# Kernel tuning notes

Measured on AMD Instinct MI355X. Metric: run time of the kernel, lower is better.

## Reference

```python
import jax, jax.numpy as jnp
import numpy as np

EPS = 1e-7  # tf.keras.backend.epsilon()
DEGREE = 5
SCALE_BASE = 1.0
SCALE_LEGENDRE = 1.0


def legendre_basis(x, degree):
    # min/max normalization over the feature axis -> x_norm in [-1, 1]
    x_min = jnp.min(x, axis=-1, keepdims=True)
    x_max = jnp.max(x, axis=-1, keepdims=True)
    x_norm = 2.0 * (x - x_min) / (x_max - x_min + EPS) - 1.0
    polys = [jnp.ones_like(x_norm), x_norm]
    for n in range(2, degree + 1):
        p_n = ((2 * n - 1) * x_norm * polys[-1] - (n - 1) * polys[-2]) / n
        polys.append(p_n)
    return jnp.stack(polys, axis=-1)  # [b, i, degree+1]


def setup_inputs() -> dict:
    key = jax.random.key(0)
    k1, k2, k3 = jax.random.split(key, 3)
    b, i, o, d = 4096, 1024, 1024, DEGREE + 1
    x = jax.random.normal(k1, (b, i), dtype=jnp.float32)
    # HeUniform: limit = sqrt(6 / fan_in)
    lim_b = np.sqrt(6.0 / i)
    base_weight = jax.random.uniform(k2, (i, o), dtype=jnp.float32, minval=-lim_b, maxval=lim_b)
    legendre_weight = jax.random.uniform(k3, (i, o, d), dtype=jnp.float32, minval=-lim_b, maxval=lim_b)
    return {"x": x, "base_weight": base_weight, "legendre_weight": legendre_weight}


def reference(x, base_weight, legendre_weight):
    base_output = jax.nn.silu(x @ base_weight)  # [b, o]
    basis = legendre_basis(x, DEGREE)  # [b, i, d]
    # 'bi,iod,bid->bo' == fold x into the basis then contract (i, d)
    xb = x[..., None] * basis  # [b, i, d]
    legendre_output = jnp.einsum('bid,iod->bo', xb, legendre_weight)
    return SCALE_BASE * base_output + SCALE_LEGENDRE * legendre_output
```

## Files before the change

kernel.cpp:

```cpp
#include <hip/hip_runtime.h>
#include <stdint.h>

typedef unsigned short u16;
typedef unsigned int   u32;
typedef __attribute__((ext_vector_type(8)))  short bhalf8;
typedef __attribute__((ext_vector_type(16))) float f32x16;

#define B_ROWS 4096
#define I_DIM  1024
#define O_DIM  1024
#define N_D    6
#define K_LEG  (I_DIM * N_D)

#define BM 256
#define BN 256
#define BK 32
#define NU 56
#define SLOT_BYTES 32768
#define LDS_BYTES  131072

__device__ __forceinline__ u16 f2b(float f) {
  u32 u = __float_as_uint(f);
  return (u16)((u + 0x7fffu + ((u >> 16) & 1u)) >> 16);
}

__device__ __forceinline__ void gld_lds16(const void* g, void* l) {
  __builtin_amdgcn_global_load_lds(
      (const __attribute__((address_space(1))) u32*)(uintptr_t)g,
      (__attribute__((address_space(3))) u32*)(u32)(uintptr_t)l, 16, 0, 0);
}

#define RS 201
__global__ void k_prep_w(const float* __restrict__ bw, const float* __restrict__ lw,
                         u16* __restrict__ Bb, u16* __restrict__ Bl) {
  __shared__ float t[32 * RS];
  if (blockIdx.x < 1024) {
    const int bx = blockIdx.x & 31, by = blockIdx.x >> 5;
    const int i0 = by * 32, o0 = bx * 32;
    const int c = threadIdx.x & 31, r0 = threadIdx.x >> 5;
    #pragma unroll
    for (int k = 0; k < 4; ++k) {
      int r = r0 + k * 8;
      t[r * 33 + c] = bw[(size_t)(i0 + r) * O_DIM + o0 + c];
    }
    __syncthreads();
    #pragma unroll
    for (int k = 0; k < 4; ++k) {
      int r = r0 + k * 8;
      Bb[(size_t)(o0 + r) * I_DIM + i0 + c] = f2b(t[c * 33 + r]);
    }
  } else {
    const int blk = blockIdx.x - 1024;
    const int bx = blk & 31, by = blk >> 5;
    const int i0 = by * 32, o0 = bx * 32;
    for (int q = threadIdx.x; q < 32 * 48; q += 256) {
      int ri = q / 48, s4 = q % 48;
      float4 v = *(const float4*)(lw + (size_t)(i0 + ri) * (O_DIM * N_D) + o0 * N_D + s4 * 4);
      float* p = t + ri * RS + s4 * 4;
      p[0] = v.x; p[1] = v.y; p[2] = v.z; p[3] = v.w;
    }
    __syncthreads();
    for (int q = threadIdx.x; q < 32 * 96; q += 256) {
      int ro = q / 96, k = q % 96;
      int e0 = 2 * k, e1 = 2 * k + 1;
      float v0 = t[(e0 / 6) * RS + ro * 6 + (e0 % 6)];
      float v1 = t[(e1 / 6) * RS + ro * 6 + (e1 % 6)];
      u32* dst = (u32*)(Bl + (size_t)(o0 + ro) * K_LEG + i0 * N_D);
      dst[k] = (u32)f2b(v0) | ((u32)f2b(v1) << 16);
    }
  }
}

__global__ void k_prep_basis(const float* __restrict__ x,
                             u16* __restrict__ Ab, u16* __restrict__ Al) {
  int b = blockIdx.x;
  int t = threadIdx.x;
  float4 v = ((const float4*)(x + (size_t)b * I_DIM))[t];
  float mn = fminf(fminf(v.x, v.y), fminf(v.z, v.w));
  float mx = fmaxf(fmaxf(v.x, v.y), fmaxf(v.z, v.w));
  #pragma unroll
  for (int off = 32; off > 0; off >>= 1) {
    mn = fminf(mn, __shfl_xor(mn, off, 64));
    mx = fmaxf(mx, __shfl_xor(mx, off, 64));
  }
  __shared__ float smn[4], smx[4];
  if ((t & 63) == 0) { smn[t >> 6] = mn; smx[t >> 6] = mx; }
  __syncthreads();
  mn = fminf(fminf(smn[0], smn[1]), fminf(smn[2], smn[3]));
  mx = fmaxf(fmaxf(smx[0], smx[1]), fmaxf(smx[2], smx[3]));
  float sc = 2.0f / (mx - mn + 1e-7f);

  float xs[4] = {v.x, v.y, v.z, v.w};
  u32 lb[12];
  #pragma unroll
  for (int e = 0; e < 4; ++e) {
    float xv = xs[e];
    float xn = (xv - mn) * sc - 1.0f;
    float p0 = 1.0f, p1 = xn;
    float p2 = (3.0f * xn * p1 - 1.0f * p0) * (1.0f / 2.0f);
    float p3 = (5.0f * xn * p2 - 2.0f * p1) * (1.0f / 3.0f);
    float p4 = (7.0f * xn * p3 - 3.0f * p2) * (1.0f / 4.0f);
    float p5 = (9.0f * xn * p4 - 4.0f * p3) * (1.0f / 5.0f);
    lb[e * 3 + 0] = (u32)f2b(xv * p0) | ((u32)f2b(xv * p1) << 16);
    lb[e * 3 + 1] = (u32)f2b(xv * p2) | ((u32)f2b(xv * p3) << 16);
    lb[e * 3 + 2] = (u32)f2b(xv * p4) | ((u32)f2b(xv * p5) << 16);
  }
  u32 a0 = (u32)f2b(xs[0]) | ((u32)f2b(xs[1]) << 16);
  u32 a1 = (u32)f2b(xs[2]) | ((u32)f2b(xs[3]) << 16);
  *(uint2*)(Ab + (size_t)b * I_DIM + t * 4) = make_uint2(a0, a1);
  uint4* dl = (uint4*)(Al + (size_t)b * K_LEG + t * 24);
  dl[0] = make_uint4(lb[0], lb[1], lb[2], lb[3]);
  dl[1] = make_uint4(lb[4], lb[5], lb[6], lb[7]);
  dl[2] = make_uint4(lb[8], lb[9], lb[10], lb[11]);
}

__global__ __launch_bounds__(512, 2) void k_gemm(
    const u16* __restrict__ Ab, const u16* __restrict__ Bb,
    const u16* __restrict__ Al, const u16* __restrict__ Bl,
    float* __restrict__ out, float* __restrict__ P) {
  extern __shared__ char lds[];

  const int tid  = threadIdx.x;
  const int wave = tid >> 6;
  const int lane = tid & 63;
  const int wm = wave >> 2;
  const int wn = wave & 3;
  const u32 lr = lane & 31;
  const u32 hi = (u32)lane >> 5;

  const int bid   = blockIdx.x;
  const int bx    = bid >> 4;
  const int by    = (bid >> 2) & 3;
  const int split = bid & 3;
  const size_t brow = (size_t)bx * BM;
  const size_t bcol = (size_t)by * BN;
  const bool s0 = (split == 0);
  const int legbase = s0 ? 0 : (24 + 56 * (split - 1));

  const int r4 = tid >> 2;
  const u32 skey = (((u32)r4 >> 1) & 3) ^ (((u32)r4 >> 3) & 3);
  const size_t cs = (size_t)(((u32)(tid & 3) ^ skey) * 8);
  char* const l0 = lds + (u32)wave * 1024;

  const u16 *gA0, *gA1, *gB0, *gB1;
  auto set_ptrs = [&](const u16* A, const u16* Bt, size_t ldk, size_t kt) {
    const size_t ko = kt * BK + cs;
    gA0 = A  + (brow + r4) * ldk + ko;
    gA1 = A  + (brow + 128 + r4) * ldk + ko;
    gB0 = Bt + (bcol + r4) * ldk + ko;
    gB1 = Bt + (bcol + 128 + r4) * ldk + ko;
  };
  if (s0) set_ptrs(Ab, Bb, I_DIM, 0);
  else    set_ptrs(Al, Bl, K_LEG, (size_t)legbase);

  auto stage = [&](int v) {
    if (s0 && v == 32) set_ptrs(Al, Bl, K_LEG, 0);
    char* d = l0 + (size_t)(v & 3) * SLOT_BYTES;
    gld_lds16(gA0, d);          gld_lds16(gA1, d + 8192);
    gld_lds16(gB0, d + 16384);  gld_lds16(gB1, d + 24576);
    gA0 += BK; gA1 += BK; gB0 += BK; gB1 += BK;
  };

  const u32 key = ((lr >> 1) & 3) ^ ((lr >> 3) & 3);
  const u32 c00 = ((0 + hi) ^ key) * 16;
  const u32 c10 = ((2 + hi) ^ key) * 16;
  const u32 abase_r = (u32)wm * 8192 + lr * 64;
  const u32 bbase_r = 16384u + ((u32)wn >> 1) * 8192 + ((u32)wn & 1) * 4096 + lr * 64;

  f32x16 acc[4][2] = {};
  bhalf8 a0[4], b0[2], a1[4], b1[2], a2[4], b2[2];

  auto silu = [&]() {
    #pragma unroll
    for (int m = 0; m < 4; ++m)
      #pragma unroll
      for (int n = 0; n < 2; ++n)
        #pragma unroll
        for (int j = 0; j < 16; ++j) {
          float v = acc[m][n][j];
          acc[m][n][j] = v / (1.0f + __expf(-v));
        }
  };

#define FILL(u1, CH, AA, BB) do {                                             \
    const char* pn_ = lds + (size_t)((u1) & 3) * SLOT_BYTES;                  \
    BB[0] = *(const bhalf8*)(pn_ + bbase_r + (CH));                           \
    BB[1] = *(const bhalf8*)(pn_ + bbase_r + 2048 + (CH));                    \
    AA[0] = *(const bhalf8*)(pn_ + abase_r + (CH));                           \
    AA[1] = *(const bhalf8*)(pn_ + abase_r + 2048 + (CH));                    \
    AA[2] = *(const bhalf8*)(pn_ + abase_r + 4096 + (CH));                    \
    AA[3] = *(const bhalf8*)(pn_ + abase_r + 6144 + (CH));                    \
  } while (0)

#define MM(AA, BB) do {                                                       \
    __builtin_amdgcn_sched_barrier(0);                                        \
    __builtin_amdgcn_s_setprio(1);                                            \
    _Pragma("unroll")                                                         \
    for (int m = 0; m < 4; ++m)                                               \
      _Pragma("unroll")                                                       \
      for (int n = 0; n < 2; ++n)                                             \
        acc[m][n] = __builtin_amdgcn_mfma_f32_32x32x16_bf16(AA[m], BB[n], acc[m][n], 0, 0, 0); \
    __builtin_amdgcn_s_setprio(0);                                            \
    __builtin_amdgcn_sched_barrier(0);                                        \
  } while (0)

#define TILE(u, PA, PB, QA, QB, RA, RB) do {                                  \
    const int u_ = (u);                                                       \
    if (s0 && u_ == 32) silu();                                               \
    if (u_ <= NU - 3) {                                                       \
      stage(u_ + 2);                                                          \
      asm volatile("s_waitcnt vmcnt(4)" ::: "memory");   \
    } else {                                                                  \
      asm volatile("s_waitcnt vmcnt(0)" ::: "memory");                        \
    }                                                                         \
    __builtin_amdgcn_s_barrier();                                             \
    if (u_ < NU - 1) FILL(u_ + 1, c00, RA, RB);                               \
    MM(PA, PB);                                                               \
    if (u_ < NU - 1) FILL(u_ + 1, c10, PA, PB);                               \
    MM(QA, QB);                                                               \
  } while (0)

  stage(0); stage(1);
  asm volatile("s_waitcnt vmcnt(4)" ::: "memory");
  __builtin_amdgcn_s_barrier();
  FILL(0, c00, a0, b0);
  FILL(0, c10, a1, b1);

  for (int t = 0; t < 18; ++t) {
    const int u = t * 3;
    TILE(u,     a0, b0, a1, b1, a2, b2);
    TILE(u + 1, a2, b2, a0, b0, a1, b1);
    TILE(u + 2, a1, b1, a2, b2, a0, b0);
  }
  TILE(54, a0, b0, a1, b1, a2, b2);
  TILE(55, a2, b2, a0, b0, a1, b1);
#undef TILE
#undef MM
#undef FILL

  float* dst = s0 ? out : (P + (size_t)(split - 1) * ((size_t)B_ROWS * O_DIM));
  #pragma unroll
  for (int m = 0; m < 4; ++m)
    #pragma unroll
    for (int n = 0; n < 2; ++n) {
      const size_t rb = brow + wm * 128 + m * 32 + 4 * hi;
      const size_t c  = bcol + wn * 64 + n * 32 + lr;
      #pragma unroll
      for (int j = 0; j < 16; ++j) {
        const size_t r = rb + (j & 3) + 8 * (j >> 2);
        dst[r * O_DIM + c] = acc[m][n][j];
      }
    }
}

__global__ void k_reduce(float* __restrict__ out, const float* __restrict__ P) {
  const size_t i = (size_t)blockIdx.x * 256 + threadIdx.x;
  const size_t NE = (size_t)B_ROWS * O_DIM / 4;
  float4 a = ((const float4*)out)[i];
  float4 b = ((const float4*)P)[i];
  float4 c = ((const float4*)P)[i + NE];
  float4 d = ((const float4*)P)[i + 2 * NE];
  a.x += b.x + c.x + d.x;  a.y += b.y + c.y + d.y;
  a.z += b.z + c.z + d.z;  a.w += b.w + c.w + d.w;
  ((float4*)out)[i] = a;
}

extern "C" void kernel_launch(void* const* d_in, const int* in_sizes, int n_in,
                              void* d_out, int out_size, void* d_ws, size_t ws_size,
                              hipStream_t stream) {
  const float* x  = (const float*)d_in[0];
  const float* bw = (const float*)d_in[1];
  const float* lw = (const float*)d_in[2];
  float* out = (float*)d_out;

  char* w = (char*)d_ws;
  u16*  Ab = (u16*)(w);
  u16*  Al = (u16*)(w + (size_t)8   * 1024 * 1024);
  u16*  Bb = (u16*)(w + (size_t)56  * 1024 * 1024);
  u16*  Bl = (u16*)(w + (size_t)58  * 1024 * 1024);
  float* P = (float*)(w + (size_t)72 * 1024 * 1024);

  hipFuncSetAttribute((const void*)k_gemm,
                      hipFuncAttributeMaxDynamicSharedMemorySize, LDS_BYTES);

  k_prep_w    <<<dim3(2048), 256, 0, stream>>>(bw, lw, Bb, Bl);
  k_prep_basis<<<dim3(B_ROWS), 256, 0, stream>>>(x, Ab, Al);
  k_gemm      <<<dim3(4 * (B_ROWS / BM) * (O_DIM / BN)), 512, LDS_BYTES, stream>>>(Ab, Bb, Al, Bl, out, P);
  k_reduce    <<<dim3((B_ROWS * O_DIM / 4) / 256), 256, 0, stream>>>(out, P);
}
```

Measured before the change: 114.1 us.

## Restructure GEMM pipeline to BK=64 double buffering and merge prep kernels

Replaces the 4-slot BK=32 triple-register-buffered pipeline with a BK=64 double-buffered LDS scheme. Each K step interleaves the next tile's global-to-LDS loads with four MFMA sub-steps, then ends with a full __syncthreads. It also merges the weight and basis prep kernels into one launch to cut launch overhead. The price is a block-wide barrier every step and only double buffering, so load latency may be less well hidden than with the previous fine-grained vmcnt waits.

```diff
diff --git a/kernel.cpp b/kernel.cpp
--- a/kernel.cpp
+++ b/kernel.cpp
@@ -14,10 +14,10 @@
 
 #define BM 256
 #define BN 256
-#define BK 32
-#define NU 56
-#define SLOT_BYTES 32768
-#define LDS_BYTES  131072
+#define BK 64
+#define NS 28
+#define BUF_BYTES 65536
+#define LDS_BYTES 131072
 
 __device__ __forceinline__ u16 f2b(float f) {
   u32 u = __float_as_uint(f);
@@ -31,8 +31,10 @@
 }
 
 #define RS 201
-__global__ void k_prep_w(const float* __restrict__ bw, const float* __restrict__ lw,
-                         u16* __restrict__ Bb, u16* __restrict__ Bl) {
+__global__ void k_prep(const float* __restrict__ bw, const float* __restrict__ lw,
+                       const float* __restrict__ x,
+                       u16* __restrict__ Bb, u16* __restrict__ Bl,
+                       u16* __restrict__ Ab, u16* __restrict__ Al) {
   __shared__ float t[32 * RS];
   if (blockIdx.x < 1024) {
     const int bx = blockIdx.x & 31, by = blockIdx.x >> 5;
@@ -49,7 +51,7 @@
       int r = r0 + k * 8;
       Bb[(size_t)(o0 + r) * I_DIM + i0 + c] = f2b(t[c * 33 + r]);
     }
-  } else {
+  } else if (blockIdx.x < 2048) {
     const int blk = blockIdx.x - 1024;
     const int bx = blk & 31, by = blk >> 5;
     const int i0 = by * 32, o0 = bx * 32;
@@ -68,50 +70,47 @@
       u32* dst = (u32*)(Bl + (size_t)(o0 + ro) * K_LEG + i0 * N_D);
       dst[k] = (u32)f2b(v0) | ((u32)f2b(v1) << 16);
     }
+  } else {
+    const int b = blockIdx.x - 2048;
+    const int tt = threadIdx.x;
+    float4 v = ((const float4*)(x + (size_t)b * I_DIM))[tt];
+    float mn = fminf(fminf(v.x, v.y), fminf(v.z, v.w));
+    float mx = fmaxf(fmaxf(v.x, v.y), fmaxf(v.z, v.w));
+    #pragma unroll
+    for (int off = 32; off > 0; off >>= 1) {
+      mn = fminf(mn, __shfl_xor(mn, off, 64));
+      mx = fmaxf(mx, __shfl_xor(mx, off, 64));
+    }
+    __shared__ float smn[4], smx[4];
+    if ((tt & 63) == 0) { smn[tt >> 6] = mn; smx[tt >> 6] = mx; }
+    __syncthreads();
+    mn = fminf(fminf(smn[0], smn[1]), fminf(smn[2], smn[3]));
+    mx = fmaxf(fmaxf(smx[0], smx[1]), fmaxf(smx[2], smx[3]));
+    float sc = 2.0f / (mx - mn + 1e-7f);
+
+    float xs[4] = {v.x, v.y, v.z, v.w};
+    u32 lb[12];
+    #pragma unroll
+    for (int e = 0; e < 4; ++e) {
+      float xv = xs[e];
+      float xn = (xv - mn) * sc - 1.0f;
+      float p0 = 1.0f, p1 = xn;
+      float p2 = (3.0f * xn * p1 - 1.0f * p0) * (1.0f / 2.0f);
+      float p3 = (5.0f * xn * p2 - 2.0f * p1) * (1.0f / 3.0f);
+      float p4 = (7.0f * xn * p3 - 3.0f * p2) * (1.0f / 4.0f);
+      float p5 = (9.0f * xn * p4 - 4.0f * p3) * (1.0f / 5.0f);
+      lb[e * 3 + 0] = (u32)f2b(xv * p0) | ((u32)f2b(xv * p1) << 16);
+      lb[e * 3 + 1] = (u32)f2b(xv * p2) | ((u32)f2b(xv * p3) << 16);
+      lb[e * 3 + 2] = (u32)f2b(xv * p4) | ((u32)f2b(xv * p5) << 16);
+    }
+    u32 a0 = (u32)f2b(xs[0]) | ((u32)f2b(xs[1]) << 16);
+    u32 a1 = (u32)f2b(xs[2]) | ((u32)f2b(xs[3]) << 16);
+    *(uint2*)(Ab + (size_t)b * I_DIM + tt * 4) = make_uint2(a0, a1);
+    uint4* dl = (uint4*)(Al + (size_t)b * K_LEG + tt * 24);
+    dl[0] = make_uint4(lb[0], lb[1], lb[2], lb[3]);
+    dl[1] = make_uint4(lb[4], lb[5], lb[6], lb[7]);
+    dl[2] = make_uint4(lb[8], lb[9], lb[10], lb[11]);
   }
-}
-
-__global__ void k_prep_basis(const float* __restrict__ x,
-                             u16* __restrict__ Ab, u16* __restrict__ Al) {
-  int b = blockIdx.x;
-  int t = threadIdx.x;
-  float4 v = ((const float4*)(x + (size_t)b * I_DIM))[t];
-  float mn = fminf(fminf(v.x, v.y), fminf(v.z, v.w));
-  float mx = fmaxf(fmaxf(v.x, v.y), fmaxf(v.z, v.w));
-  #pragma unroll
-  for (int off = 32; off > 0; off >>= 1) {
-    mn = fminf(mn, __shfl_xor(mn, off, 64));
-    mx = fmaxf(mx, __shfl_xor(mx, off, 64));
-  }
-  __shared__ float smn[4], smx[4];
-  if ((t & 63) == 0) { smn[t >> 6] = mn; smx[t >> 6] = mx; }
-  __syncthreads();
-  mn = fminf(fminf(smn[0], smn[1]), fminf(smn[2], smn[3]));
-  mx = fmaxf(fmaxf(smx[0], smx[1]), fmaxf(smx[2], smx[3]));
-  float sc = 2.0f / (mx - mn + 1e-7f);
-
-  float xs[4] = {v.x, v.y, v.z, v.w};
-  u32 lb[12];
-  #pragma unroll
-  for (int e = 0; e < 4; ++e) {
-    float xv = xs[e];
-    float xn = (xv - mn) * sc - 1.0f;
-    float p0 = 1.0f, p1 = xn;
-    float p2 = (3.0f * xn * p1 - 1.0f * p0) * (1.0f / 2.0f);
-    float p3 = (5.0f * xn * p2 - 2.0f * p1) * (1.0f / 3.0f);
-    float p4 = (7.0f * xn * p3 - 3.0f * p2) * (1.0f / 4.0f);
-    float p5 = (9.0f * xn * p4 - 4.0f * p3) * (1.0f / 5.0f);
-    lb[e * 3 + 0] = (u32)f2b(xv * p0) | ((u32)f2b(xv * p1) << 16);
-    lb[e * 3 + 1] = (u32)f2b(xv * p2) | ((u32)f2b(xv * p3) << 16);
-    lb[e * 3 + 2] = (u32)f2b(xv * p4) | ((u32)f2b(xv * p5) << 16);
-  }
-  u32 a0 = (u32)f2b(xs[0]) | ((u32)f2b(xs[1]) << 16);
-  u32 a1 = (u32)f2b(xs[2]) | ((u32)f2b(xs[3]) << 16);
-  *(uint2*)(Ab + (size_t)b * I_DIM + t * 4) = make_uint2(a0, a1);
-  uint4* dl = (uint4*)(Al + (size_t)b * K_LEG + t * 24);
-  dl[0] = make_uint4(lb[0], lb[1], lb[2], lb[3]);
-  dl[1] = make_uint4(lb[4], lb[5], lb[6], lb[7]);
-  dl[2] = make_uint4(lb[8], lb[9], lb[10], lb[11]);
 }
 
 __global__ __launch_bounds__(512, 2) void k_gemm(
@@ -125,7 +124,7 @@
   const int lane = tid & 63;
   const int wm = wave >> 2;
   const int wn = wave & 3;
-  const u32 lr = lane & 31;
+  const u32 lr = (u32)lane & 31;
   const u32 hi = (u32)lane >> 5;
 
   const int bid   = blockIdx.x;
@@ -135,108 +134,91 @@
   const size_t brow = (size_t)bx * BM;
   const size_t bcol = (size_t)by * BN;
   const bool s0 = (split == 0);
-  const int legbase = s0 ? 0 : (24 + 56 * (split - 1));
-
-  const int r4 = tid >> 2;
-  const u32 skey = (((u32)r4 >> 1) & 3) ^ (((u32)r4 >> 3) & 3);
-  const size_t cs = (size_t)(((u32)(tid & 3) ^ skey) * 8);
-  char* const l0 = lds + (u32)wave * 1024;
-
-  const u16 *gA0, *gA1, *gB0, *gB1;
-  auto set_ptrs = [&](const u16* A, const u16* Bt, size_t ldk, size_t kt) {
-    const size_t ko = kt * BK + cs;
-    gA0 = A  + (brow + r4) * ldk + ko;
-    gA1 = A  + (brow + 128 + r4) * ldk + ko;
-    gB0 = Bt + (bcol + r4) * ldk + ko;
-    gB1 = Bt + (bcol + 128 + r4) * ldk + ko;
+  const int legbase = s0 ? 0 : (12 + 28 * (split - 1));
+
+  const int rt = tid >> 3;
+  const u32 ct = (((u32)tid & 7) ^ ((u32)rt & 7)) * 8;
+
+  auto stage_half = [&](int v, int h) {
+    char* dst = lds + (size_t)(v & 1) * BUF_BYTES + ((h >= 2) ? 32768 : 0)
+              + (size_t)(h & 1) * 16384 + (size_t)tid * 16;
+    const size_t rbase = ((h < 2) ? brow : bcol) + (size_t)(h & 1) * 128 + (size_t)rt;
+    const u16* src0;
+    size_t rstep;
+    if (s0 && v < 16) {
+      const u16* M = (h < 2) ? Ab : Bb;
+      src0 = M + rbase * I_DIM + (size_t)v * BK + ct;
+      rstep = (size_t)64 * I_DIM;
+    } else {
+      const int lv = s0 ? (v - 16) : (legbase + v);
+      const u16* M = (h < 2) ? Al : Bl;
+      src0 = M + rbase * K_LEG + (size_t)lv * BK + ct;
+      rstep = (size_t)64 * K_LEG;
+    }
+    gld_lds16(src0, dst);
+    gld_lds16(src0 + rstep, dst + 8192);
   };
-  if (s0) set_ptrs(Ab, Bb, I_DIM, 0);
-  else    set_ptrs(Al, Bl, K_LEG, (size_t)legbase);
-
-  auto stage = [&](int v) {
-    if (s0 && v == 32) set_ptrs(Al, Bl, K_LEG, 0);
-    char* d = l0 + (size_t)(v & 3) * SLOT_BYTES;
-    gld_lds16(gA0, d);          gld_lds16(gA1, d + 8192);
-    gld_lds16(gB0, d + 16384);  gld_lds16(gB1, d + 24576);
-    gA0 += BK; gA1 += BK; gB0 += BK; gB1 += BK;
-  };
-
-  const u32 key = ((lr >> 1) & 3) ^ ((lr >> 3) & 3);
-  const u32 c00 = ((0 + hi) ^ key) * 16;
-  const u32 c10 = ((2 + hi) ^ key) * 16;
-  const u32 abase_r = (u32)wm * 8192 + lr * 64;
-  const u32 bbase_r = 16384u + ((u32)wn >> 1) * 8192 + ((u32)wn & 1) * 4096 + lr * 64;
+
+  const u32 c0off = (hi ^ ((u32)lane & 7)) * 16;
+  const u32 abase = ((u32)wm * 128 + lr) * 128;
+  const u32 bbase = 32768u + ((u32)wn * 64 + lr) * 128;
 
   f32x16 acc[4][2] = {};
-  bhalf8 a0[4], b0[2], a1[4], b1[2], a2[4], b2[2];
-
-  auto silu = [&]() {
-    #pragma unroll
-    for (int m = 0; m < 4; ++m)
-      #pragma unroll
-      for (int n = 0; n < 2; ++n)
-        #pragma unroll
-        for (int j = 0; j < 16; ++j) {
-          float v = acc[m][n][j];
-          acc[m][n][j] = v / (1.0f + __expf(-v));
-        }
-  };
-
-#define FILL(u1, CH, AA, BB) do {                                             \
-    const char* pn_ = lds + (size_t)((u1) & 3) * SLOT_BYTES;                  \
-    BB[0] = *(const bhalf8*)(pn_ + bbase_r + (CH));                           \
-    BB[1] = *(const bhalf8*)(pn_ + bbase_r + 2048 + (CH));                    \
-    AA[0] = *(const bhalf8*)(pn_ + abase_r + (CH));                           \
-    AA[1] = *(const bhalf8*)(pn_ + abase_r + 2048 + (CH));                    \
-    AA[2] = *(const bhalf8*)(pn_ + abase_r + 4096 + (CH));                    \
-    AA[3] = *(const bhalf8*)(pn_ + abase_r + 6144 + (CH));                    \
+  bhalf8 afa[4], bfa[2], afb[4], bfb[2];
+
+#define READF(AF, BF, P_, KK) do {                                            \
+    const u32 co_ = c0off ^ ((KK) << 5);                                      \
+    BF[0] = *(const bhalf8*)((P_) + bbase + co_);                             \
+    BF[1] = *(const bhalf8*)((P_) + bbase + 4096 + co_);                      \
+    AF[0] = *(const bhalf8*)((P_) + abase + co_);                             \
+    AF[1] = *(const bhalf8*)((P_) + abase + 4096 + co_);                      \
+    AF[2] = *(const bhalf8*)((P_) + abase + 8192 + co_);                      \
+    AF[3] = *(const bhalf8*)((P_) + abase + 12288 + co_);                     \
   } while (0)
 
-#define MM(AA, BB) do {                                                       \
-    __builtin_amdgcn_sched_barrier(0);                                        \
+#define MM(AF, BF) do {                                                       \
     __builtin_amdgcn_s_setprio(1);                                            \
     _Pragma("unroll")                                                         \
     for (int m = 0; m < 4; ++m)                                               \
       _Pragma("unroll")                                                       \
       for (int n = 0; n < 2; ++n)                                             \
-        acc[m][n] = __builtin_amdgcn_mfma_f32_32x32x16_bf16(AA[m], BB[n], acc[m][n], 0, 0, 0); \
+        acc[m][n] = __builtin_amdgcn_mfma_f32_32x32x16_bf16(AF[m], BF[n], acc[m][n], 0, 0, 0); \
     __builtin_amdgcn_s_setprio(0);                                            \
-    __builtin_amdgcn_sched_barrier(0);                                        \
   } while (0)
 
-#define TILE(u, PA, PB, QA, QB, RA, RB) do {                                  \
-    const int u_ = (u);                                                       \
-    if (s0 && u_ == 32) silu();                                               \
-    if (u_ <= NU - 3) {                                                       \
-      stage(u_ + 2);                                                          \
-      asm volatile("s_waitcnt vmcnt(4)" ::: "memory");   \
-    } else {                                                                  \
-      asm volatile("s_waitcnt vmcnt(0)" ::: "memory");                        \
-    }                                                                         \
-    __builtin_amdgcn_s_barrier();                                             \
-    if (u_ < NU - 1) FILL(u_ + 1, c00, RA, RB);                               \
-    MM(PA, PB);                                                               \
-    if (u_ < NU - 1) FILL(u_ + 1, c10, PA, PB);                               \
-    MM(QA, QB);                                                               \
-  } while (0)
-
-  stage(0); stage(1);
-  asm volatile("s_waitcnt vmcnt(4)" ::: "memory");
-  __builtin_amdgcn_s_barrier();
-  FILL(0, c00, a0, b0);
-  FILL(0, c10, a1, b1);
-
-  for (int t = 0; t < 18; ++t) {
-    const int u = t * 3;
-    TILE(u,     a0, b0, a1, b1, a2, b2);
-    TILE(u + 1, a2, b2, a0, b0, a1, b1);
-    TILE(u + 2, a1, b1, a2, b2, a0, b0);
+  stage_half(0, 0); stage_half(0, 1); stage_half(0, 2); stage_half(0, 3);
+  __syncthreads();
+
+  for (int u = 0; u < NS; ++u) {
+    if (s0 && u == 16) {
+      #pragma unroll
+      for (int m = 0; m < 4; ++m)
+        #pragma unroll
+        for (int n = 0; n < 2; ++n)
+          #pragma unroll
+          for (int j = 0; j < 16; ++j) {
+            float v = acc[m][n][j];
+            acc[m][n][j] = v / (1.0f + __expf(-v));
+          }
+    }
+    const char* p = lds + (size_t)(u & 1) * BUF_BYTES;
+    const bool st = (u < NS - 1);
+    READF(afa, bfa, p, 0);
+    if (st) stage_half(u + 1, 0);
+    READF(afb, bfb, p, 1);
+    MM(afa, bfa);
+    if (st) stage_half(u + 1, 1);
+    READF(afa, bfa, p, 2);
+    MM(afb, bfb);
+    if (st) stage_half(u + 1, 2);
+    READF(afb, bfb, p, 3);
+    MM(afa, bfa);
+    if (st) stage_half(u + 1, 3);
+    MM(afb, bfb);
+    __syncthreads();
   }
-  TILE(54, a0, b0, a1, b1, a2, b2);
-  TILE(55, a2, b2, a0, b0, a1, b1);
-#undef TILE
+#undef READF
 #undef MM
-#undef FILL
 
   float* dst = s0 ? out : (P + (size_t)(split - 1) * ((size_t)B_ROWS * O_DIM));
   #pragma unroll
@@ -283,8 +265,7 @@
   hipFuncSetAttribute((const void*)k_gemm,
                       hipFuncAttributeMaxDynamicSharedMemorySize, LDS_BYTES);
 
-  k_prep_w    <<<dim3(2048), 256, 0, stream>>>(bw, lw, Bb, Bl);
-  k_prep_basis<<<dim3(B_ROWS), 256, 0, stream>>>(x, Ab, Al);
-  k_gemm      <<<dim3(4 * (B_ROWS / BM) * (O_DIM / BN)), 512, LDS_BYTES, stream>>>(Ab, Bb, Al, Bl, out, P);
-  k_reduce    <<<dim3((B_ROWS * O_DIM / 4) / 256), 256, 0, stream>>>(out, P);
-}
+  k_prep  <<<dim3(2048 + B_ROWS), 256, 0, stream>>>(bw, lw, x, Bb, Bl, Ab, Al);
+  k_gemm  <<<dim3(4 * (B_ROWS / BM) * (O_DIM / BN)), 512, LDS_BYTES, stream>>>(Ab, Bb, Al, Bl, out, P);
+  k_reduce<<<dim3((B_ROWS * O_DIM / 4) / 256), 256, 0, stream>>>(out, P);
+}
```

New measurement: 108.5 us. 1.05x faster.
